# Kernel tuning notes

Measured on AMD Instinct MI355X. Metric: run time of the kernel, lower is better.

Reference implementation:

```python
import jax, jax.numpy as jnp
import numpy as np

N_ORB = 1024    # Monte-Carlo orbits
NTIMES = 1024   # observation epochs
N_FZ = 24       # zodi flux grid points (uniform in log10)
N_KEZ = 6       # exozodi multipliers (sorted, searchsorted lookup)
N_TINT = 64     # integration times
N_ALPHA = 512   # separations (uniform in log10)


def setup_inputs() -> dict:
    key = jax.random.key(0)
    k1, k2, k3, k4 = jax.random.split(key, 4)
    fZs = jnp.logspace(-10.0, -7.0, N_FZ).astype(jnp.float32)
    alphas = jnp.logspace(-2.0, 1.0, N_ALPHA).astype(jnp.float32)
    kEZs = jnp.array([0.5, 1.0, 2.0, 5.0, 10.0, 20.0], dtype=jnp.float32)
    # grid already in the module's internal (n_fZ, n_kEZ, n_tint, n_alpha) layout
    grid = 25.0 + jax.random.normal(k1, (N_FZ, N_KEZ, N_TINT, N_ALPHA), dtype=jnp.float32)
    # alpha slightly exceeds [alphas[0], alphas[-1]] so geom_mask is exercised
    alpha = (10.0 ** jax.random.uniform(k2, (N_ORB, NTIMES), minval=-2.2, maxval=1.1)).astype(jnp.float32)
    dMag = (25.0 + jax.random.normal(k3, (N_ORB, NTIMES))).astype(jnp.float32)
    fZ_vals = (10.0 ** jax.random.uniform(k4, (NTIMES,), minval=-10.0, maxval=-7.0)).astype(jnp.float32)
    kEZ_val = jnp.float32(1.5)
    return dict(alpha=alpha, dMag=dMag, fZ_vals=fZ_vals, kEZ_val=kEZ_val,
                grid=grid, fZs=fZs, kEZs=kEZs, alphas=alphas)


def reference(alpha, dMag, fZ_vals, kEZ_val, grid, fZs, kEZs, alphas):
    """Faithful vectorized translation of dMag0Grid._pdet_alpha_dMag.

    alpha, dMag: (n_orb, ntimes); fZ_vals: (ntimes,); kEZ_val: scalar;
    grid: (n_fZ, n_kEZ, n_tint, n_alpha). Returns pdet (ntimes, n_tint).
    """
    n_fZ = fZs.shape[0]
    n_alpha = alphas.shape[0]
    log_fZs = jnp.log10(fZs)
    inv_log_fZ_step = 1.0 / (log_fZs[1] - log_fZs[0])
    log_alphas = jnp.log10(alphas)
    inv_log_alpha_step = 1.0 / (log_alphas[1] - log_alphas[0])

    geom_mask = (alpha >= alphas[0]) & (alpha <= alphas[-1])          # (n_orb, ntimes)

    fZ_ind = (jnp.log10(fZ_vals) - log_fZs[0]) * inv_log_fZ_step
    fZ0 = jnp.clip(jnp.floor(fZ_ind).astype(jnp.int32) + 1, 0, n_fZ - 2)  # (ntimes,)

    a_ind = (jnp.log10(alpha) - log_alphas[0]) * inv_log_alpha_step
    a0 = jnp.clip(a_ind.astype(jnp.int32), 0, n_alpha - 1)               # (n_orb, ntimes)
    dalpha = (a_ind - a0).astype(grid.dtype)

    kEZ_ind = jnp.searchsorted(kEZs, kEZ_val, side='right') - 1

    # lax.dynamic_slice clamps the start so the width-2 window fits:
    s = jnp.minimum(a0, n_alpha - 2)                                     # (n_orb, ntimes)

    g = jnp.take(grid, kEZ_ind, axis=1)                                  # (n_fZ, n_tint, n_alpha)
    g_f = g[fZ0]                                                          # (ntimes, n_tint, n_alpha)
    sT = s.T                                                              # (ntimes, n_orb)
    g0 = jnp.take_along_axis(g_f, sT[:, None, :], axis=2)                 # (ntimes, n_tint, n_orb)
    g1 = jnp.take_along_axis(g_f, (sT + 1)[:, None, :], axis=2)
    res = g0 + dalpha.T[:, None, :] * (g1 - g0)                           # (ntimes, n_tint, n_orb)

    dim = jnp.transpose(res, (2, 0, 1))                                   # (n_orb, ntimes, n_tint)
    det_mask = geom_mask[..., None] & jnp.signbit(dMag[..., None] - dim)
    pdet = det_mask.astype(jnp.float32).mean(axis=0)                      # (ntimes, n_tint)
    return pdet
```

## Files before the change

### kernel.cpp

```cpp
#include <hip/hip_runtime.h>
#include <math.h>

#define N_ORB   1024
#define NTIMES  1024
#define N_FZ    24
#define N_KEZ   6
#define N_TINT  64
#define N_ALPHA 512

#define GT_BYTES (N_FZ * N_ALPHA * N_TINT * 4)

__global__ __launch_bounds__(256) void transpose_grid(
    const float* __restrict__ grid, const float* __restrict__ kEZs,
    const float* __restrict__ kEZ_val_p, float* __restrict__ gT)
{
    __shared__ float tile[64 * 65];

    float kv = kEZ_val_p[0];
    int cnt = 0;
#pragma unroll
    for (int i = 0; i < N_KEZ; ++i) cnt += (kEZs[i] <= kv) ? 1 : 0;
    int kez = cnt - 1;
    kez = kez < 0 ? 0 : (kez > N_KEZ - 1 ? N_KEZ - 1 : kez);

    int fz   = blockIdx.x;
    int sc   = blockIdx.y;
    int w    = threadIdx.x >> 6;
    int lane = threadIdx.x & 63;

    const float* gsrc = grid + ((size_t)fz * N_KEZ + kez) * N_TINT * N_ALPHA;

#pragma unroll
    for (int r = 0; r < 16; ++r) {
        int tint = w * 16 + r;
        tile[tint * 65 + lane] = gsrc[(size_t)tint * N_ALPHA + sc * 64 + lane];
    }
    __syncthreads();
#pragma unroll
    for (int r = 0; r < 16; ++r) {
        int sl = w * 16 + r;
        gT[((size_t)fz * N_ALPHA + sc * 64 + sl) * N_TINT + lane] = tile[lane * 65 + sl];
    }
}

__global__ __launch_bounds__(256) void prep_orbits(
    const float* __restrict__ alpha, const float* __restrict__ dMag,
    const float* __restrict__ alphas, float4* __restrict__ P)
{
    __shared__ float da_t[64 * 65];
    __shared__ float dm_t[64 * 65];
    __shared__ int   of_t[64 * 65];

    float al0 = alphas[0], al1 = alphas[N_ALPHA - 1];
    float la0 = log10f(al0);
    float inv_step = 1.0f / (log10f(alphas[1]) - la0);

    int o0 = blockIdx.y * 64, t0 = blockIdx.x * 64;
    int w = threadIdx.x >> 6, lane = threadIdx.x & 63;

#pragma unroll
    for (int r = 0; r < 16; ++r) {
        int ol = w * 16 + r;
        size_t idx = (size_t)(o0 + ol) * NTIMES + t0 + lane;
        float a = alpha[idx];
        float d = dMag[idx];
        float a_ind = (log10f(a) - la0) * inv_step;
        int a0i = (int)a_ind;
        a0i = a0i < 0 ? 0 : (a0i > N_ALPHA - 1 ? N_ALPHA - 1 : a0i);
        float dal = a_ind - (float)a0i;
        int s = a0i > N_ALPHA - 2 ? N_ALPHA - 2 : a0i;
        bool geom = (a >= al0) && (a <= al1);
        da_t[ol * 65 + lane] = dal;
        dm_t[ol * 65 + lane] = geom ? d : __builtin_inff();
        of_t[ol * 65 + lane] = s * N_TINT;
    }
    __syncthreads();
#pragma unroll
    for (int r = 0; r < 16; ++r) {
        int tl = w * 16 + r;
        float4 v;
        v.x = da_t[lane * 65 + tl];
        v.y = dm_t[lane * 65 + tl];
        v.z = __int_as_float(of_t[lane * 65 + tl]);
        v.w = 0.0f;
        P[(size_t)(t0 + tl) * N_ORB + o0 + lane] = v;
    }
}

__global__ __launch_bounds__(256) void pdet_main(
    const float* __restrict__ fZ_vals, const float* __restrict__ fZs,
    const float* __restrict__ gT, const float4* __restrict__ P,
    float* __restrict__ out)
{
    __shared__ int red[4 * 64];

    int t = blockIdx.x;
    float lf0 = log10f(fZs[0]);
    float inv_f = 1.0f / (log10f(fZs[1]) - lf0);
    float fi = (log10f(fZ_vals[t]) - lf0) * inv_f;
    int f0 = (int)floorf(fi) + 1;
    f0 = f0 < 0 ? 0 : (f0 > N_FZ - 2 ? N_FZ - 2 : f0);

    const float*  gB = gT + (size_t)f0 * N_ALPHA * N_TINT;
    const float4* Pt = P + (size_t)t * N_ORB;

    int w = threadIdx.x >> 6, lane = threadIdx.x & 63;
    int q = lane >> 4;
    int tg = (lane & 15) << 2;

    int c0 = 0, c1 = 0, c2 = 0, c3 = 0;
    int ob = w * 256 + q;

#pragma unroll 4
    for (int it = 0; it < 64; ++it) {
        float4 pd = Pt[ob + it * 4];
        float dal = pd.x, dm = pd.y;
        int offw = __float_as_int(pd.z);
        const float4* row = reinterpret_cast<const float4*>(gB + offw + tg);
        float4 g0 = row[0];
        float4 g1 = row[16];
        c0 += dm < fmaf(dal, g1.x - g0.x, g0.x);
        c1 += dm < fmaf(dal, g1.y - g0.y, g0.y);
        c2 += dm < fmaf(dal, g1.z - g0.z, g0.z);
        c3 += dm < fmaf(dal, g1.w - g0.w, g0.w);
    }

    c0 += __shfl_xor(c0, 16); c0 += __shfl_xor(c0, 32);
    c1 += __shfl_xor(c1, 16); c1 += __shfl_xor(c1, 32);
    c2 += __shfl_xor(c2, 16); c2 += __shfl_xor(c2, 32);
    c3 += __shfl_xor(c3, 16); c3 += __shfl_xor(c3, 32);

    if (lane < 16) {
        red[w * 64 + lane * 4 + 0] = c0;
        red[w * 64 + lane * 4 + 1] = c1;
        red[w * 64 + lane * 4 + 2] = c2;
        red[w * 64 + lane * 4 + 3] = c3;
    }
    __syncthreads();
    if (threadIdx.x < 64) {
        int tot = red[threadIdx.x] + red[64 + threadIdx.x] +
                  red[128 + threadIdx.x] + red[192 + threadIdx.x];
        out[(size_t)t * N_TINT + threadIdx.x] = (float)tot * (1.0f / 1024.0f);
    }
}

extern "C" void kernel_launch(void* const* d_in, const int* in_sizes, int n_in,
                              void* d_out, int out_size, void* d_ws, size_t ws_size,
                              hipStream_t stream) {
    const float* alpha   = (const float*)d_in[0];
    const float* dMag    = (const float*)d_in[1];
    const float* fZ_vals = (const float*)d_in[2];
    const float* kEZ_val = (const float*)d_in[3];
    const float* grid    = (const float*)d_in[4];
    const float* fZs     = (const float*)d_in[5];
    const float* kEZs    = (const float*)d_in[6];
    const float* alphas  = (const float*)d_in[7];
    float*  out = (float*)d_out;

    float*  gT = (float*)d_ws;
    float4* P  = (float4*)((char*)d_ws + GT_BYTES);

    transpose_grid<<<dim3(N_FZ, N_ALPHA / 64), 256, 0, stream>>>(grid, kEZs, kEZ_val, gT);
    prep_orbits<<<dim3(NTIMES / 64, N_ORB / 64), 256, 0, stream>>>(alpha, dMag, alphas, P);
    pdet_main<<<dim3(NTIMES), 256, 0, stream>>>(fZ_vals, fZs, gT, P, out);
}
```

Before: 115.2 us.

## Counting-sort orbits by alpha bin in LDS and skip geometry-masked orbits

Each block loads its epoch's 1024 orbit records into LDS and counting-sorts them by alpha slot, sending masked orbits (infinite dMag) to a last bin. The main loop then walks only the alive orbits in sorted order, so neighbouring wavefronts read nearby grid rows for better cache locality and masked orbits are never processed. This adds histogram atomics, a prefix scan, several barriers and 16KB of LDS per block, which may lower occupancy. The loop count now varies per block, which can leave the main loop somewhat unbalanced across blocks.

Result: faster. 108.1 us (-6.1%).

```diff
diff --git a/kernel.cpp b/kernel.cpp
--- a/kernel.cpp
+++ b/kernel.cpp
@@ -92,9 +92,16 @@
     const float* __restrict__ gT, const float4* __restrict__ P,
     float* __restrict__ out)
 {
-    __shared__ int red[4 * 64];
+    __shared__ float4 Psort[N_ORB];
+    __shared__ int    hist[512];
+    __shared__ int    histPS[512];
+    __shared__ int    red[4 * 64];
+    __shared__ int    aliveLDS;
 
     int t = blockIdx.x;
+    int tid = threadIdx.x;
+    int w = tid >> 6, lane = tid & 63;
+
     float lf0 = log10f(fZs[0]);
     float inv_f = 1.0f / (log10f(fZs[1]) - lf0);
     float fi = (log10f(fZ_vals[t]) - lf0) * inv_f;
@@ -104,16 +111,57 @@
     const float*  gB = gT + (size_t)f0 * N_ALPHA * N_TINT;
     const float4* Pt = P + (size_t)t * N_ORB;
 
-    int w = threadIdx.x >> 6, lane = threadIdx.x & 63;
-    int q = lane >> 4;
+    hist[tid] = 0; hist[tid + 256] = 0;
+    __syncthreads();
+
+    float4 v[4];
+    int    bin[4];
+#pragma unroll
+    for (int k = 0; k < 4; ++k) {
+        v[k] = Pt[tid + k * 256];
+        int s = __float_as_int(v[k].z) >> 6;
+        bin[k] = isinf(v[k].y) ? 511 : s;
+        atomicAdd(&hist[bin[k]], 1);
+    }
+    __syncthreads();
+
+    if (tid < 64) {
+        int pre[8]; int run = 0;
+#pragma unroll
+        for (int j = 0; j < 8; ++j) { pre[j] = run; run += hist[tid * 8 + j]; }
+        int inc = run;
+#pragma unroll
+        for (int d = 1; d < 64; d <<= 1) {
+            int n = __shfl_up(inc, d);
+            if (lane >= d) inc += n;
+        }
+        int excl = inc - run;
+#pragma unroll
+        for (int j = 0; j < 8; ++j) histPS[tid * 8 + j] = excl + pre[j];
+        if (tid == 63) aliveLDS = excl + pre[7] + hist[511] - hist[511];
+        if (tid == 63) aliveLDS = excl + pre[7];
+    }
+    __syncthreads();
+
+#pragma unroll
+    for (int k = 0; k < 4; ++k) {
+        int pos = atomicAdd(&histPS[bin[k]], 1);
+        Psort[pos] = v[k];
+    }
+    __syncthreads();
+
+    int alive = aliveLDS;
+    int nIter = (alive + 15) >> 4;
+
+    int q  = lane >> 4;
     int tg = (lane & 15) << 2;
+    int sid = w * 4 + q;
 
     int c0 = 0, c1 = 0, c2 = 0, c3 = 0;
-    int ob = w * 256 + q;
 
 #pragma unroll 4
-    for (int it = 0; it < 64; ++it) {
-        float4 pd = Pt[ob + it * 4];
+    for (int it = 0; it < nIter; ++it) {
+        float4 pd = Psort[it * 16 + sid];
         float dal = pd.x, dm = pd.y;
         int offw = __float_as_int(pd.z);
         const float4* row = reinterpret_cast<const float4*>(gB + offw + tg);
@@ -137,10 +185,9 @@
         red[w * 64 + lane * 4 + 3] = c3;
     }
     __syncthreads();
-    if (threadIdx.x < 64) {
-        int tot = red[threadIdx.x] + red[64 + threadIdx.x] +
-                  red[128 + threadIdx.x] + red[192 + threadIdx.x];
-        out[(size_t)t * N_TINT + threadIdx.x] = (float)tot * (1.0f / 1024.0f);
+    if (tid < 64) {
+        int tot = red[tid] + red[64 + tid] + red[128 + tid] + red[192 + tid];
+        out[(size_t)t * N_TINT + tid] = (float)tot * (1.0f / 1024.0f);
     }
 }
 
```
